# Performance work log

Measured on AMD Instinct MI355X. Metric: run time of the kernel, lower is better.

Reference implementation:

```python
import jax, jax.numpy as jnp
import numpy as np

TOP_K = 2

def setup_inputs() -> dict:
    key = jax.random.key(0)
    ks = jax.random.split(key, 8)
    B, S, H, I, E = 1, 2048, 2048, 8192, 8
    s = 0.02
    return {
        "hidden_states": jax.random.normal(ks[0], (B, S, H), jnp.float32),
        "gate_w": jax.random.normal(ks[1], (H, E), jnp.float32) * s,
        "gate_b": jnp.zeros((E,), jnp.float32),
        "fc1_w": jax.random.normal(ks[2], (E, H, I), jnp.float32) * s,
        "fc1_b": jnp.zeros((E, I), jnp.float32),
        "fc2_w": jax.random.normal(ks[3], (E, I, H), jnp.float32) * s,
        "fc2_b": jnp.zeros((E, H), jnp.float32),
        "alpha": jax.random.normal(ks[4], (E,), jnp.float32),
    }

def reference(hidden_states, gate_w, gate_b, fc1_w, fc1_b, fc2_w, fc2_b, alpha):
    B, S, H = hidden_states.shape
    E = alpha.shape[0]
    x = hidden_states.reshape(-1, H)  # [T, H]

    # GShard-style gate: linear -> softmax -> top-k
    logits = x @ gate_w + gate_b              # [T, E]
    scores = jax.nn.softmax(logits, axis=-1)  # [T, E]
    top_v, top_i = jax.lax.top_k(scores, TOP_K)  # [T, K]

    # Dense per-token combine weight per expert: sum_k onehot(idx_k) * score_k, scaled by alpha[e]
    gates = jnp.sum(jax.nn.one_hot(top_i, E, dtype=x.dtype) * top_v[..., None], axis=1)  # [T, E]
    gates = gates * alpha[None, :]

    # Per-expert MLP applied to all tokens (math identical to masked dispatch+combine)
    h1 = jax.nn.gelu(jnp.einsum('th,ehi->eti', x, fc1_w) + fc1_b[:, None, :], approximate=True)  # [E, T, I]
    out_all = jnp.einsum('eti,eih->eth', h1, fc2_w) + fc2_b[:, None, :]                          # [E, T, H]
    out = jnp.einsum('eth,te->th', out_all, gates)  # weighted combine [T, H]
    return out.reshape(B, S, H)
```

## Files before the change

kernel.cpp:

```cpp
#include <hip/hip_runtime.h>
#include <hip/hip_bf16.h>
#include <cstdint>

#define T_TOK 2048
#define HDIM  2048
#define IDIM  8192
#define NEXP  8

typedef short s16x8 __attribute__((ext_vector_type(8)));
typedef float f32x4 __attribute__((ext_vector_type(4)));
typedef const __attribute__((address_space(1))) uint32_t gbl_u32;
typedef __attribute__((address_space(3))) uint32_t lds_u32;

__device__ __forceinline__ unsigned short f2b(float f) {
    union { float f; unsigned u; } c; c.f = f;
    unsigned r = (c.u + 0x7fffu + ((c.u >> 16) & 1u)) >> 16;
    return (unsigned short)r;
}

__device__ __forceinline__ float gelu_tanh(float v) {
    float u = 0.7978845608028654f * (v + 0.044715f * v * v * v);
    return 0.5f * v * (1.0f + tanhf(u));
}

__global__ __launch_bounds__(256) void k_gate(
    const float* __restrict__ x, const float* __restrict__ gw,
    const float* __restrict__ gb, const float* __restrict__ alpha,
    unsigned short* __restrict__ xb, int* __restrict__ counts,
    int* __restrict__ top_e, float* __restrict__ top_g)
{
    const int wave = threadIdx.x >> 6;
    const int lane = threadIdx.x & 63;
    const int t = blockIdx.x * 4 + wave;
    if (t >= T_TOK) return;

    float acc[8];
    #pragma unroll
    for (int e = 0; e < 8; e++) acc[e] = 0.f;

    const float* xrow = x + (size_t)t * HDIM;
    unsigned short* xbrow = xb + (size_t)t * HDIM;

    #pragma unroll
    for (int c = 0; c < 8; c++) {
        const int h0 = c * 256 + lane * 4;
        const float4 xv = *reinterpret_cast<const float4*>(xrow + h0);
        ushort4 u;
        u.x = f2b(xv.x); u.y = f2b(xv.y); u.z = f2b(xv.z); u.w = f2b(xv.w);
        *reinterpret_cast<ushort4*>(xbrow + h0) = u;
        const float xs[4] = {xv.x, xv.y, xv.z, xv.w};
        #pragma unroll
        for (int r = 0; r < 4; r++) {
            const float4 g0 = *reinterpret_cast<const float4*>(gw + (size_t)(h0 + r) * 8);
            const float4 g1 = *reinterpret_cast<const float4*>(gw + (size_t)(h0 + r) * 8 + 4);
            acc[0] += xs[r] * g0.x; acc[1] += xs[r] * g0.y;
            acc[2] += xs[r] * g0.z; acc[3] += xs[r] * g0.w;
            acc[4] += xs[r] * g1.x; acc[5] += xs[r] * g1.y;
            acc[6] += xs[r] * g1.z; acc[7] += xs[r] * g1.w;
        }
    }
    #pragma unroll
    for (int e = 0; e < 8; e++) {
        #pragma unroll
        for (int off = 32; off > 0; off >>= 1)
            acc[e] += __shfl_xor(acc[e], off);
        acc[e] += gb[e];
    }
    float m = acc[0];
    #pragma unroll
    for (int e = 1; e < 8; e++) m = fmaxf(m, acc[e]);
    float Z = 0.f;
    #pragma unroll
    for (int e = 0; e < 8; e++) Z += expf(acc[e] - m);
    int e0 = 0; float b0 = acc[0];
    #pragma unroll
    for (int e = 1; e < 8; e++) if (acc[e] > b0) { b0 = acc[e]; e0 = e; }
    int e1 = -1; float b1 = -1e30f;
    #pragma unroll
    for (int e = 0; e < 8; e++) if (e != e0 && acc[e] > b1) { b1 = acc[e]; e1 = e; }

    if (lane == 0) {
        const float s0 = expf(b0 - m) / Z * alpha[e0];
        const float s1 = expf(b1 - m) / Z * alpha[e1];
        top_e[2 * t]     = e0; top_e[2 * t + 1] = e1;
        top_g[2 * t]     = s0; top_g[2 * t + 1] = s1;
        atomicAdd(&counts[e0], 1);
        atomicAdd(&counts[e1], 1);
    }
}

__global__ void k_scan(const int* __restrict__ counts, int* __restrict__ offsets,
                       int* __restrict__ cursors)
{
    if (threadIdx.x == 0) {
        int off = 0;
        for (int e = 0; e < NEXP; e++) {
            offsets[e] = off; cursors[e] = off; off += counts[e];
        }
    }
}

__global__ __launch_bounds__(256) void k_append(
    const int* __restrict__ top_e, const float* __restrict__ top_g,
    int* __restrict__ cursors, int* __restrict__ slot_token,
    float* __restrict__ slot_gate, int* __restrict__ tok2slot)
{
    const int t = blockIdx.x * 256 + threadIdx.x;
    if (t >= T_TOK) return;
    #pragma unroll
    for (int k = 0; k < 2; k++) {
        const int e = top_e[2 * t + k];
        const int slot = atomicAdd(&cursors[e], 1);
        slot_token[slot] = t;
        slot_gate[slot]  = top_g[2 * t + k];
        tok2slot[2 * t + k] = slot;
    }
}

__global__ __launch_bounds__(256) void k_convT(
    const float* __restrict__ W, unsigned short* __restrict__ WT,
    int KW, int NW)
{
    const int e  = blockIdx.z;
    const int k0 = blockIdx.y * 128;
    const int n0 = blockIdx.x * 64;
    const float* src = W + (size_t)e * KW * NW;
    unsigned short* dst = WT + (size_t)e * KW * NW;

    __shared__ unsigned short lt[64][136];

    const int tid = threadIdx.x;
    const int n4 = (tid & 15) * 4;
    #pragma unroll
    for (int r = 0; r < 8; r++) {
        const int kr = (tid >> 4) + r * 16;
        const float4 v = *reinterpret_cast<const float4*>(
            src + (size_t)(k0 + kr) * NW + n0 + n4);
        lt[n4 + 0][kr] = f2b(v.x);
        lt[n4 + 1][kr] = f2b(v.y);
        lt[n4 + 2][kr] = f2b(v.z);
        lt[n4 + 3][kr] = f2b(v.w);
    }
    __syncthreads();
    const int n  = tid >> 2;
    const int kc = (tid & 3) * 32;
    unsigned short* orow = dst + (size_t)(n0 + n) * KW + k0 + kc;
    const uint4* lsrc = reinterpret_cast<const uint4*>(&lt[n][kc]);
    #pragma unroll
    for (int i = 0; i < 4; i++)
        *reinterpret_cast<uint4*>(orow + i * 8) = lsrc[i];
}

template<bool FC1>
__global__ __launch_bounds__(256, 4) void k_gemm(
    const unsigned short* __restrict__ Abase,
    const unsigned short* __restrict__ WT,
    const float* __restrict__ bias,
    const int* __restrict__ counts,
    const int* __restrict__ offsets,
    const int* __restrict__ slot_token,
    const float* __restrict__ slot_gate,
    unsigned short* __restrict__ out_bf,
    float* __restrict__ out_f)
{
    constexpr int N  = FC1 ? IDIM : HDIM;
    constexpr int K  = FC1 ? HDIM : IDIM;
    constexpr int BN = FC1 ? 128 : 64;
    constexpr int NT = N / BN;
    constexpr int MT = T_TOK / 128;
    constexpr int NK = K / 64;
    constexpr int MI = FC1 ? 4 : 2;
    constexpr int BITS = BN / 32;

    constexpr int nwg = NEXP * NT * MT;
    constexpr int cpx = nwg >> 3;
    const int bid = blockIdx.x;
    const int wg  = (bid & 7) * cpx + (bid >> 3);
    const int e   = wg / (NT * MT);
    const int rem = wg - e * (NT * MT);
    const int nb  = rem / MT;
    const int mb  = rem - nb * MT;

    const int cnt = counts[e];
    const int m0  = mb * 128;
    if (m0 >= cnt) return;
    const int moff  = offsets[e];
    const int n0    = nb * BN;
    const int slot0 = moff + m0;

    __shared__ short As[128 * 64];
    __shared__ short Bs[BN * 64];

    const int tid  = threadIdx.x;
    const int lane = tid & 63, wave = tid >> 6;
    const int lo = lane & 15, hi = lane >> 4;
    const int wmb = FC1 ? (wave >> 1) * 64 : wave * 32;
    const int wnb = FC1 ? (wave & 1) * 64 : 0;

    const unsigned short* asrc[4];
    #pragma unroll
    for (int it = 0; it < 4; it++) {
        const int row = (tid >> 3) + it * 32;
        int tok;
        if (FC1) tok = (m0 + row < cnt) ? slot_token[moff + m0 + row] : 0;
        else     tok = slot0 + ((m0 + row < cnt) ? row : 0);
        asrc[it] = Abase + (size_t)tok * K;
    }
    const unsigned short* bsrc[BITS];
    #pragma unroll
    for (int it = 0; it < BITS; it++) {
        const int row = (tid >> 3) + it * 32;
        bsrc[it] = WT + (size_t)e * (size_t)N * K + (size_t)(n0 + row) * K;
    }
    const int achunk = tid & 7;

    f32x4 acc[MI][4];
    #pragma unroll
    for (int i = 0; i < MI; i++)
        #pragma unroll
        for (int j = 0; j < 4; j++) acc[i][j] = (f32x4)0.f;

    for (int t = 0; t < NK; t++) {
        const int kk = t * 64;
        #pragma unroll
        for (int it = 0; it < 4; it++) {
            const int row = (tid >> 3) + it * 32;
            const int sc  = achunk ^ (row & 7);
            __builtin_amdgcn_global_load_lds(
                (gbl_u32*)(asrc[it] + kk + sc * 8),
                (lds_u32*)(As + (tid + it * 256) * 8), 16, 0, 0);
        }
        #pragma unroll
        for (int it = 0; it < BITS; it++) {
            const int row = (tid >> 3) + it * 32;
            const int sc  = achunk ^ (row & 7);
            __builtin_amdgcn_global_load_lds(
                (gbl_u32*)(bsrc[it] + kk + sc * 8),
                (lds_u32*)(Bs + (tid + it * 256) * 8), 16, 0, 0);
        }
        __syncthreads();
        #pragma unroll
        for (int ks = 0; ks < 2; ks++) {
            s16x8 af[MI], bfr[4];
            #pragma unroll
            for (int i = 0; i < MI; i++) {
                const int arow = wmb + i * 16 + lo;
                const int ch = (ks * 4 + hi) ^ (arow & 7);
                af[i] = *reinterpret_cast<const s16x8*>(As + arow * 64 + ch * 8);
            }
            #pragma unroll
            for (int j = 0; j < 4; j++) {
                const int brow = wnb + j * 16 + lo;
                const int ch = (ks * 4 + hi) ^ (brow & 7);
                bfr[j] = *reinterpret_cast<const s16x8*>(Bs + brow * 64 + ch * 8);
            }
            __builtin_amdgcn_s_setprio(1);
            #pragma unroll
            for (int i = 0; i < MI; i++)
                #pragma unroll
                for (int j = 0; j < 4; j++)
                    acc[i][j] = __builtin_amdgcn_mfma_f32_16x16x32_bf16(
                        af[i], bfr[j], acc[i][j], 0, 0, 0);
            __builtin_amdgcn_s_setprio(0);
        }
        __syncthreads();
    }

    #pragma unroll
    for (int i = 0; i < MI; i++) {
        #pragma unroll
        for (int r = 0; r < 4; r++) {
            const int row = wmb + i * 16 + hi * 4 + r;
            if (m0 + row >= cnt) continue;
            if (FC1) {
                const size_t orow = (size_t)(slot0 + row) * IDIM;
                #pragma unroll
                for (int j = 0; j < 4; j++) {
                    const int col = n0 + wnb + j * 16 + lo;
                    const float v = acc[i][j][r] + bias[e * N + col];
                    out_bf[orow + col] = f2b(gelu_tanh(v));
                }
            } else {
                const float g = slot_gate[slot0 + row];
                const size_t orow = (size_t)(slot0 + row) * HDIM;
                #pragma unroll
                for (int j = 0; j < 4; j++) {
                    const int col = n0 + wnb + j * 16 + lo;
                    out_f[orow + col] = g * (acc[i][j][r] + bias[e * N + col]);
                }
            }
        }
    }
}

__global__ __launch_bounds__(256) void k_combine(
    const float* __restrict__ outslot, const int* __restrict__ tok2slot,
    float* __restrict__ out)
{
    const int t = blockIdx.x;
    const int sA = tok2slot[2 * t], sB = tok2slot[2 * t + 1];
    const float* ra = outslot + (size_t)sA * HDIM;
    const float* rb = outslot + (size_t)sB * HDIM;
    float* ro = out + (size_t)t * HDIM;
    #pragma unroll
    for (int c = 0; c < 2; c++) {
        const int i = c * 1024 + threadIdx.x * 4;
        const float4 a = *reinterpret_cast<const float4*>(ra + i);
        const float4 b = *reinterpret_cast<const float4*>(rb + i);
        float4 o; o.x = a.x + b.x; o.y = a.y + b.y; o.z = a.z + b.z; o.w = a.w + b.w;
        *reinterpret_cast<float4*>(ro + i) = o;
    }
}

extern "C" void kernel_launch(void* const* d_in, const int* in_sizes, int n_in,
                              void* d_out, int out_size, void* d_ws, size_t ws_size,
                              hipStream_t stream)
{
    const float* x  = (const float*)d_in[0];
    const float* gw = (const float*)d_in[1];
    const float* gb = (const float*)d_in[2];
    const float* w1 = (const float*)d_in[3];
    const float* b1 = (const float*)d_in[4];
    const float* w2 = (const float*)d_in[5];
    const float* b2 = (const float*)d_in[6];
    const float* al = (const float*)d_in[7];
    float* out = (float*)d_out;

    char* ws = (char*)d_ws;
    unsigned short* xb  = (unsigned short*)ws;
    unsigned short* h1  = (unsigned short*)(ws + 8388608);
    float* outslot      = (float*)(ws + 75497472);
    unsigned short* wT1 = (unsigned short*)(ws + 109051904);
    unsigned short* wT2 = (unsigned short*)(ws + 377487360);
    char* meta = ws + 645922816;
    int* counts     = (int*)meta;
    int* offsets    = (int*)(meta + 32);
    int* cursors    = (int*)(meta + 64);
    int* slot_token = (int*)(meta + 256);
    int* tok2slot   = (int*)(meta + 256 + 16384);
    int* top_e      = (int*)(meta + 256 + 32768);
    float* slot_gate= (float*)(meta + 256 + 49152);
    float* top_g    = (float*)(meta + 256 + 65536);

    hipMemsetAsync(counts, 0, 32, stream);
    k_gate<<<dim3(T_TOK / 4), dim3(256), 0, stream>>>(x, gw, gb, al, xb, counts, top_e, top_g);
    k_scan<<<dim3(1), dim3(64), 0, stream>>>(counts, offsets, cursors);
    k_append<<<dim3(T_TOK / 256), dim3(256), 0, stream>>>(top_e, top_g, cursors,
                                                          slot_token, slot_gate, tok2slot);
    k_convT<<<dim3(IDIM / 64, HDIM / 128, NEXP), dim3(256), 0, stream>>>(w1, wT1, HDIM, IDIM);
    k_gemm<true><<<dim3(NEXP * (IDIM / 128) * (T_TOK / 128)), dim3(256), 0, stream>>>(
        xb, wT1, b1, counts, offsets, slot_token, slot_gate, h1, nullptr);
    k_convT<<<dim3(HDIM / 64, IDIM / 128, NEXP), dim3(256), 0, stream>>>(w2, wT2, IDIM, HDIM);
    k_gemm<false><<<dim3(NEXP * (HDIM / 64) * (T_TOK / 128)), dim3(256), 0, stream>>>(
        h1, wT2, b2, counts, offsets, slot_token, slot_gate, nullptr, outslot);
    k_combine<<<dim3(T_TOK), dim3(256), 0, stream>>>(outslot, tok2slot, out);
}
```

Measured before the change: 1.004 ms.

## Triple-buffer LDS tiles with K=32 steps and async prefetch in expert GEMM

```diff
diff --git a/kernel.cpp b/kernel.cpp
--- a/kernel.cpp
+++ b/kernel.cpp
@@ -152,7 +152,7 @@
 }
 
 template<bool FC1>
-__global__ __launch_bounds__(256, 4) void k_gemm(
+__global__ __launch_bounds__(256, 3) void k_gemm(
     const unsigned short* __restrict__ Abase,
     const unsigned short* __restrict__ WT,
     const float* __restrict__ bias,
@@ -168,9 +168,9 @@
     constexpr int BN = FC1 ? 128 : 64;
     constexpr int NT = N / BN;
     constexpr int MT = T_TOK / 128;
-    constexpr int NK = K / 64;
+    constexpr int NK = K / 32;
     constexpr int MI = FC1 ? 4 : 2;
-    constexpr int BITS = BN / 32;
+    constexpr int BITS = BN / 64;
 
     constexpr int nwg = NEXP * NT * MT;
     constexpr int cpx = nwg >> 3;
@@ -188,8 +188,8 @@
     const int n0    = nb * BN;
     const int slot0 = moff + m0;
 
-    __shared__ short As[128 * 64];
-    __shared__ short Bs[BN * 64];
+    __shared__ short As[3][128 * 32];
+    __shared__ short Bs[3][BN * 32];
 
     const int tid  = threadIdx.x;
     const int lane = tid & 63, wave = tid >> 6;
@@ -197,10 +197,10 @@
     const int wmb = FC1 ? (wave >> 1) * 64 : wave * 32;
     const int wnb = FC1 ? (wave & 1) * 64 : 0;
 
-    const unsigned short* asrc[4];
-    #pragma unroll
-    for (int it = 0; it < 4; it++) {
-        const int row = (tid >> 3) + it * 32;
+    const unsigned short* asrc[2];
+    #pragma unroll
+    for (int it = 0; it < 2; it++) {
+        const int row = (tid >> 2) + it * 64;
         int tok;
         if (FC1) tok = (m0 + row < cnt) ? slot_token[moff + m0 + row] : 0;
         else     tok = slot0 + ((m0 + row < cnt) ? row : 0);
@@ -209,10 +209,30 @@
     const unsigned short* bsrc[BITS];
     #pragma unroll
     for (int it = 0; it < BITS; it++) {
-        const int row = (tid >> 3) + it * 32;
+        const int row = (tid >> 2) + it * 64;
         bsrc[it] = WT + (size_t)e * (size_t)N * K + (size_t)(n0 + row) * K;
     }
-    const int achunk = tid & 7;
+
+    auto stage = [&](short* Ad, short* Bd, int kk) {
+        #pragma unroll
+        for (int it = 0; it < 2; it++) {
+            const int slot = tid + it * 256;
+            const int row = slot >> 2, c = slot & 3;
+            const int g = c ^ ((row >> 1) & 3);
+            __builtin_amdgcn_global_load_lds(
+                (gbl_u32*)(asrc[it] + kk + g * 8),
+                (lds_u32*)(Ad + slot * 8), 16, 0, 0);
+        }
+        #pragma unroll
+        for (int it = 0; it < BITS; it++) {
+            const int slot = tid + it * 256;
+            const int row = slot >> 2, c = slot & 3;
+            const int g = c ^ ((row >> 1) & 3);
+            __builtin_amdgcn_global_load_lds(
+                (gbl_u32*)(bsrc[it] + kk + g * 8),
+                (lds_u32*)(Bd + slot * 8), 16, 0, 0);
+        }
+    };
 
     f32x4 acc[MI][4];
     #pragma unroll
@@ -220,50 +240,51 @@
         #pragma unroll
         for (int j = 0; j < 4; j++) acc[i][j] = (f32x4)0.f;
 
+    auto compute = [&](const short* Ac, const short* Bc) {
+        s16x8 af[MI], bfr[4];
+        #pragma unroll
+        for (int i = 0; i < MI; i++) {
+            const int arow = wmb + i * 16 + lo;
+            const int ch = hi ^ ((arow >> 1) & 3);
+            af[i] = *reinterpret_cast<const s16x8*>(Ac + arow * 32 + ch * 8);
+        }
+        #pragma unroll
+        for (int j = 0; j < 4; j++) {
+            const int brow = wnb + j * 16 + lo;
+            const int ch = hi ^ ((brow >> 1) & 3);
+            bfr[j] = *reinterpret_cast<const s16x8*>(Bc + brow * 32 + ch * 8);
+        }
+        __builtin_amdgcn_s_setprio(1);
+        #pragma unroll
+        for (int i = 0; i < MI; i++)
+            #pragma unroll
+            for (int j = 0; j < 4; j++)
+                acc[i][j] = __builtin_amdgcn_mfma_f32_16x16x32_bf16(
+                    af[i], bfr[j], acc[i][j], 0, 0, 0);
+        __builtin_amdgcn_s_setprio(0);
+    };
+
+    auto wait_gl = []() {
+        if constexpr (FC1) asm volatile("s_waitcnt vmcnt(4)" ::: "memory");
+        else               asm volatile("s_waitcnt vmcnt(3)" ::: "memory");
+    };
+
+    short *a0 = As[0], *a1 = As[1], *a2 = As[2];
+    short *b0 = Bs[0], *b1 = Bs[1], *b2 = Bs[2];
+
+    stage(a0, b0, 0);
+    stage(a1, b1, 32);
+    wait_gl();
+    __builtin_amdgcn_s_barrier();
+
     for (int t = 0; t < NK; t++) {
-        const int kk = t * 64;
-        #pragma unroll
-        for (int it = 0; it < 4; it++) {
-            const int row = (tid >> 3) + it * 32;
-            const int sc  = achunk ^ (row & 7);
-            __builtin_amdgcn_global_load_lds(
-                (gbl_u32*)(asrc[it] + kk + sc * 8),
-                (lds_u32*)(As + (tid + it * 256) * 8), 16, 0, 0);
-        }
-        #pragma unroll
-        for (int it = 0; it < BITS; it++) {
-            const int row = (tid >> 3) + it * 32;
-            const int sc  = achunk ^ (row & 7);
-            __builtin_amdgcn_global_load_lds(
-                (gbl_u32*)(bsrc[it] + kk + sc * 8),
-                (lds_u32*)(Bs + (tid + it * 256) * 8), 16, 0, 0);
-        }
-        __syncthreads();
-        #pragma unroll
-        for (int ks = 0; ks < 2; ks++) {
-            s16x8 af[MI], bfr[4];
-            #pragma unroll
-            for (int i = 0; i < MI; i++) {
-                const int arow = wmb + i * 16 + lo;
-                const int ch = (ks * 4 + hi) ^ (arow & 7);
-                af[i] = *reinterpret_cast<const s16x8*>(As + arow * 64 + ch * 8);
-            }
-            #pragma unroll
-            for (int j = 0; j < 4; j++) {
-                const int brow = wnb + j * 16 + lo;
-                const int ch = (ks * 4 + hi) ^ (brow & 7);
-                bfr[j] = *reinterpret_cast<const s16x8*>(Bs + brow * 64 + ch * 8);
-            }
-            __builtin_amdgcn_s_setprio(1);
-            #pragma unroll
-            for (int i = 0; i < MI; i++)
-                #pragma unroll
-                for (int j = 0; j < 4; j++)
-                    acc[i][j] = __builtin_amdgcn_mfma_f32_16x16x32_bf16(
-                        af[i], bfr[j], acc[i][j], 0, 0, 0);
-            __builtin_amdgcn_s_setprio(0);
-        }
-        __syncthreads();
+        if (t + 2 < NK) stage(a2, b2, (t + 2) * 32);
+        compute(a0, b0);
+        if (t + 2 < NK)      wait_gl();
+        else if (t + 1 < NK) asm volatile("s_waitcnt vmcnt(0)" ::: "memory");
+        if (t + 1 < NK) __builtin_amdgcn_s_barrier();
+        short* ta = a0; a0 = a1; a1 = a2; a2 = ta;
+        short* tb = b0; b0 = b1; b1 = b2; b2 = tb;
     }
 
     #pragma unroll
```

New measurement: 1.103 ms. 1.1x slower.
